# Performance work log

Measured on AMD Instinct MI355X. Metric: run time of the kernel, lower is better.

## Reference

```python
import jax, jax.numpy as jnp
import numpy as np

N = 50000       # nodes
E_RAND = 800000 # random edges (avg degree ~16)
K = 64          # edges touching `node`; setup_inputs guarantees exactly K
F = 64          # num_node_features
C = 64          # conv_channels


def setup_inputs() -> dict:
    key = jax.random.key(0)
    ks = jax.random.split(key, 6)
    x = jax.random.normal(ks[0], (N, F), dtype=jnp.float32)
    # random edges avoiding node 0 so exactly the K prepended edges touch node 0
    src = jax.random.randint(ks[1], (E_RAND,), 1, N, dtype=jnp.int64)
    dst = jax.random.randint(ks[2], (E_RAND,), 1, N, dtype=jnp.int64)
    ksrc = jnp.zeros((K,), dtype=jnp.int64)
    kdst = jnp.arange(1, K + 1, dtype=jnp.int64)
    edge_index = jnp.stack([jnp.concatenate([ksrc, src]),
                            jnp.concatenate([kdst, dst])])  # [2, K+E_RAND]
    W1 = jax.random.normal(ks[3], (F, C), jnp.float32) / np.float32(np.sqrt(F))
    b1 = jnp.zeros((C,), jnp.float32)
    W2 = jax.random.normal(ks[4], (C, C), jnp.float32) / np.float32(np.sqrt(C))
    b2 = jnp.zeros((C,), jnp.float32)
    Wr = jax.random.normal(ks[5], (C, 1), jnp.float32) / np.float32(np.sqrt(C))
    br = jnp.zeros((1,), jnp.float32)
    return {"x": x, "edge_index": edge_index, "node": 0,
            "W1": W1, "b1": b1, "W2": W2, "b2": b2, "Wr": Wr, "br": br}


def gcn_conv(x, src, dst, W, b):
    """PyG GCNConv with self-loops already appended to (src, dst).
    out[v] = sum_{(u,v)} deg(u)^-1/2 * deg(v)^-1/2 * (x @ W)[u] + b
    """
    n = x.shape[0]
    xw = x @ W                                              # [N, C]
    deg = jnp.zeros((n,), xw.dtype).at[dst].add(1.0)        # in-degree incl. self-loop
    dinv = jnp.where(deg > 0, jax.lax.rsqrt(deg), 0.0)
    norm = dinv[src] * dinv[dst]                            # [E]
    out = jax.ops.segment_sum(xw[src] * norm[:, None], dst, num_segments=n)
    return out + b


def reference(x, edge_index, node, W1, b1, W2, b2, Wr, br):
    n = x.shape[0]
    loop = jnp.arange(n, dtype=edge_index.dtype)
    src = jnp.concatenate([edge_index[0], loop])  # add self loops (GCNConv default)
    dst = jnp.concatenate([edge_index[1], loop])
    h = jax.nn.relu(gcn_conv(x, src, dst, W1, b1))
    h = jax.nn.relu(gcn_conv(h, src, dst, W2, b2))
    # edges incident to `node` (setup guarantees exactly K such edges)
    s0, d0 = edge_index[0], edge_index[1]
    mask = (s0 == node) | (d0 == node)
    idx = jnp.nonzero(mask, size=K)[0]
    s, d = s0[idx], d0[idx]
    targets = jnp.where(s == node, d, s)  # self-loop (s==d==node) -> node
    score = h[targets] @ Wr + br          # [K, 1]
    score = jax.nn.softmax(score, axis=0)
    return score[:, 0], targets
```

## Files before the change

kernel.cpp:

```cpp
#include <hip/hip_runtime.h>
#include <math.h>

#define KK 64
#define CAP 64
#define NF 4160
#define BMW 1568

__device__ __forceinline__ int fnode_of(int i, const int* tsorted, const int* towner,
                                        const int* tcnt2, const int* tslots) {
    int tp = i / 65, j = i % 65;
    if (j == 0) return tsorted[tp];
    int own = towner[tp];
    int c = tcnt2[own]; if (c > CAP) c = CAP;
    return (j - 1 < c) ? tslots[own * CAP + (j - 1)] : -1;
}

__global__ __launch_bounds__(256) void k_find(const int* __restrict__ ei, int E,
                                              const int* __restrict__ nodep,
                                              int4* __restrict__ zbase, int zcount4,
                                              int* __restrict__ tcount,
                                              int* __restrict__ tpairs) {
    int idx = blockIdx.x * 256 + threadIdx.x;
    if (idx < zcount4) zbase[idx] = make_int4(0, 0, 0, 0);
    int node = nodep[0];
    int n4 = E >> 2;
    if (idx < n4) {
        int4 ss = ((const int4*)ei)[idx];
        int4 dd = ((const int4*)(ei + E))[idx];
        int s[4] = {ss.x, ss.y, ss.z, ss.w};
        int d[4] = {dd.x, dd.y, dd.z, dd.w};
#pragma unroll
        for (int k = 0; k < 4; k++) {
            if (s[k] == node || d[k] == node) {
                int q = atomicAdd(tcount, 1);
                if (q < KK) { int e = idx * 4 + k; tpairs[2 * q] = e; tpairs[2 * q + 1] = (s[k] == node) ? d[k] : s[k]; }
            }
        }
    }
    if (idx == 0) {
        for (int e = n4 * 4; e < E; e++) {
            int s = ei[e], d = ei[E + e];
            if (s == node || d == node) {
                int q = atomicAdd(tcount, 1);
                if (q < KK) { tpairs[2 * q] = e; tpairs[2 * q + 1] = (s == node) ? d : s; }
            }
        }
    }
}

__global__ __launch_bounds__(256) void k_collect_t(const int* __restrict__ ei, int E,
                                                   const int* __restrict__ tpairs,
                                                   int* __restrict__ cnt,
                                                   int* __restrict__ tcnt2,
                                                   int* __restrict__ tslots,
                                                   int* __restrict__ fmapRow,
                                                   int* __restrict__ tsorted_g,
                                                   int* __restrict__ towner_g) {
    __shared__ unsigned int bmask[BMW];
    __shared__ int tnode[KK];
    __shared__ int eidx[KK], tgt[KK], srt[KK];
    int tid = threadIdx.x;
    for (int i = tid; i < BMW; i += 256) bmask[i] = 0u;
    if (tid < KK) { eidx[tid] = tpairs[2 * tid]; tgt[tid] = tpairs[2 * tid + 1]; }
    __syncthreads();
    if (tid < KK) {
        int rank = 0;
        for (int j = 0; j < KK; j++) rank += (eidx[j] < eidx[tid]) ? 1 : 0;
        srt[rank] = tgt[tid];
    }
    __syncthreads();
    if (tid < KK) {
        int mynode = srt[tid];
        int owner = tid;
        for (int j = 0; j < tid; j++) if (srt[j] == mynode) { owner = j; break; }
        tnode[tid] = (owner == tid) ? mynode : -1;
        if (owner == tid) atomicOr(&bmask[mynode >> 5], 1u << (mynode & 31));
        if (blockIdx.x == 0) {
            tsorted_g[tid] = mynode; towner_g[tid] = owner;
            if (owner == tid) atomicCAS(&fmapRow[mynode], 0, tid * 65 + 0 + 1);
        }
    }
    __syncthreads();
    int n4 = E >> 2;
    for (int idx = blockIdx.x * 256 + tid; idx < n4; idx += gridDim.x * 256) {
        int4 ss = ((const int4*)ei)[idx];
        int4 dd = ((const int4*)(ei + E))[idx];
        int s[4] = {ss.x, ss.y, ss.z, ss.w};
        int d[4] = {dd.x, dd.y, dd.z, dd.w};
        atomicAdd(&cnt[d[0]], 1);
        atomicAdd(&cnt[d[1]], 1);
#pragma unroll
        for (int k = 0; k < 4; k++) {
            if ((bmask[d[k] >> 5] >> (d[k] & 31)) & 1u) {
                int f = 0;
                for (int j = 0; j < KK; j++) if (tnode[j] == d[k]) { f = j + 1; break; }
                if (f) {
                    int p = atomicAdd(&tcnt2[f - 1], 1);
                    if (p < CAP) {
                        tslots[(f - 1) * CAP + p] = s[k];
                        atomicCAS(&fmapRow[s[k]], 0, (f - 1) * 65 + (p + 1) + 1);
                    }
                }
            }
        }
    }
    if (blockIdx.x == 0 && tid == 0) {
        for (int e = n4 * 4; e < E; e++) {
            int d = ei[E + e];
            atomicAdd(&cnt[d], 1);
            if ((bmask[d >> 5] >> (d & 31)) & 1u) {
                int f = 0;
                for (int j = 0; j < KK; j++) if (tnode[j] == d) { f = j + 1; break; }
                if (f) {
                    int p = atomicAdd(&tcnt2[f - 1], 1);
                    if (p < CAP) {
                        tslots[(f - 1) * CAP + p] = ei[e];
                        atomicCAS(&fmapRow[ei[e]], 0, (f - 1) * 65 + (p + 1) + 1);
                    }
                }
            }
        }
    }
}

__global__ __launch_bounds__(256) void k_collect_f(const int* __restrict__ ei, int E,
                                                   const int* __restrict__ fmapRow,
                                                   int* __restrict__ cnt,
                                                   int* __restrict__ fcnt,
                                                   int* __restrict__ fslots,
                                                   const int* __restrict__ tsorted,
                                                   const int* __restrict__ towner,
                                                   const int* __restrict__ tcnt2,
                                                   const int* __restrict__ tslots,
                                                   int* __restrict__ ownerCount,
                                                   int2* __restrict__ owners) {
    int idx = blockIdx.x * 256 + threadIdx.x;
    if (idx < NF) {
        int u = fnode_of(idx, tsorted, towner, tcnt2, tslots);
        if (u >= 0 && fmapRow[u] == idx + 1) {
            int p = atomicAdd(ownerCount, 1);
            owners[p] = make_int2(idx, u);
        }
    }
    int n4 = E >> 2;
    if (idx < n4) {
        int4 ss = ((const int4*)ei)[idx];
        int4 dd = ((const int4*)(ei + E))[idx];
        atomicAdd(&cnt[dd.z], 1);
        atomicAdd(&cnt[dd.w], 1);
        int r0 = fmapRow[dd.x], r1 = fmapRow[dd.y], r2 = fmapRow[dd.z], r3 = fmapRow[dd.w];
        if (r0) { int p = atomicAdd(&fcnt[r0 - 1], 1); if (p < CAP) fslots[(size_t)(r0 - 1) * CAP + p] = ss.x; }
        if (r1) { int p = atomicAdd(&fcnt[r1 - 1], 1); if (p < CAP) fslots[(size_t)(r1 - 1) * CAP + p] = ss.y; }
        if (r2) { int p = atomicAdd(&fcnt[r2 - 1], 1); if (p < CAP) fslots[(size_t)(r2 - 1) * CAP + p] = ss.z; }
        if (r3) { int p = atomicAdd(&fcnt[r3 - 1], 1); if (p < CAP) fslots[(size_t)(r3 - 1) * CAP + p] = ss.w; }
    }
    if (idx == 0) {
        for (int e = n4 * 4; e < E; e++) {
            int r = fmapRow[ei[E + e]];
            if (r) { int p = atomicAdd(&fcnt[r - 1], 1); if (p < CAP) fslots[(size_t)(r - 1) * CAP + p] = ei[e]; }
        }
    }
}

__global__ __launch_bounds__(256) void k_layer1(const float* __restrict__ x,
                                                const int2* __restrict__ owners,
                                                const int* __restrict__ ownerCount,
                                                const int* __restrict__ cnt,
                                                const int* __restrict__ fcnt,
                                                const int* __restrict__ fslots,
                                                const float* __restrict__ W1,
                                                const float* __restrict__ b1,
                                                float* __restrict__ h1s) {
    __shared__ __align__(16) float W1s[64 * 64];
    int tid = threadIdx.x;
    int nown = ownerCount[0];
    int ngrp = (nown + 3) >> 2;
    if ((int)blockIdx.x >= ngrp) return;
    for (int j = tid; j < 1024; j += 256) ((float4*)W1s)[j] = ((const float4*)W1)[j];
    __syncthreads();
    int lane = tid & 63;
    for (int g = blockIdx.x; g < ngrp; g += gridDim.x) {
        int idx = g * 4 + (tid >> 6);
        if (idx >= nown) continue;
        int2 ou = owners[idx];
        int i = ou.x, u = ou.y;
        float du = rsqrtf((float)(cnt[u] + 1));
        float acc = du * x[(size_t)u * 64 + lane];
        int c = fcnt[i]; if (c > CAP) c = CAP;
        const int* sl = fslots + (size_t)i * CAP;
        int k = 0;
        for (; k + 4 <= c; k += 4) {
            int u0 = sl[k], u1 = sl[k + 1], u2 = sl[k + 2], u3 = sl[k + 3];
            float f0 = rsqrtf((float)(cnt[u0] + 1));
            float f1 = rsqrtf((float)(cnt[u1] + 1));
            float f2 = rsqrtf((float)(cnt[u2] + 1));
            float f3 = rsqrtf((float)(cnt[u3] + 1));
            acc += f0 * x[(size_t)u0 * 64 + lane] + f1 * x[(size_t)u1 * 64 + lane]
                 + f2 * x[(size_t)u2 * 64 + lane] + f3 * x[(size_t)u3 * 64 + lane];
        }
        for (; k < c; k++) {
            int uu = sl[k];
            acc += rsqrtf((float)(cnt[uu] + 1)) * x[(size_t)uu * 64 + lane];
        }
        float z = du * acc;
        float h = 0.f;
#pragma unroll
        for (int f = 0; f < 64; f++) h += __shfl(z, f) * W1s[f * 64 + lane];
        h = fmaxf(h + b1[lane], 0.f);
        h1s[(size_t)i * 64 + lane] = du * h;
    }
}

__global__ __launch_bounds__(64) void k_score2(const float* __restrict__ h1s,
                                               const int* __restrict__ tsorted,
                                               const int* __restrict__ towner,
                                               const int* __restrict__ tcnt2,
                                               const int* __restrict__ tslots,
                                               const int* __restrict__ fmapRow,
                                               const int* __restrict__ cnt,
                                               const float* __restrict__ W2,
                                               const float* __restrict__ b2,
                                               const float* __restrict__ Wr,
                                               float* __restrict__ sc,
                                               int* __restrict__ done,
                                               float* __restrict__ out) {
    int tp = blockIdx.x;
    int lane = threadIdx.x;
    int t = tsorted[tp];
    float dt = rsqrtf((float)(cnt[t] + 1));
    int own = towner[tp];
    int c = tcnt2[own]; if (c > CAP) c = CAP;
    const int* sl = tslots + own * CAP;
    float z = h1s[(size_t)(fmapRow[t] - 1) * 64 + lane];
#pragma unroll 8
    for (int j = 0; j < c; j++) {
        int u = sl[j];
        int row = fmapRow[u] - 1;
        z += h1s[(size_t)row * 64 + lane];
    }
    z *= dt;
    float acc = 0.f;
#pragma unroll
    for (int f = 0; f < 64; f++) acc += __shfl(z, f) * W2[f * 64 + lane];
    float h2 = fmaxf(acc + b2[lane], 0.f);
    float p = h2 * Wr[lane];
#pragma unroll
    for (int off = 32; off >= 1; off >>= 1) p += __shfl_xor(p, off);
    int last = 0;
    if (lane == 0) {
        __hip_atomic_store(&sc[tp], p, __ATOMIC_RELEASE, __HIP_MEMORY_SCOPE_AGENT);
        last = (__hip_atomic_fetch_add(done, 1, __ATOMIC_ACQ_REL, __HIP_MEMORY_SCOPE_AGENT) == KK - 1) ? 1 : 0;
    }
    last = __shfl(last, 0);
    if (last) {
        float s = __hip_atomic_load(&sc[lane], __ATOMIC_ACQUIRE, __HIP_MEMORY_SCOPE_AGENT);
        float m = s;
#pragma unroll
        for (int off = 32; off >= 1; off >>= 1) m = fmaxf(m, __shfl_xor(m, off));
        float e = __expf(s - m);
        float ssum = e;
#pragma unroll
        for (int off = 32; off >= 1; off >>= 1) ssum += __shfl_xor(ssum, off);
        out[lane] = e / ssum;
        out[KK + lane] = (float)tsorted[lane];
    }
}

extern "C" void kernel_launch(void* const* d_in, const int* in_sizes, int n_in,
                              void* d_out, int out_size, void* d_ws, size_t ws_size,
                              hipStream_t stream) {
    const float* x  = (const float*)d_in[0];
    const int*   ei = (const int*)d_in[1];
    const int*   nodep = (const int*)d_in[2];
    const float* W1 = (const float*)d_in[3];
    const float* b1 = (const float*)d_in[4];
    const float* W2 = (const float*)d_in[5];
    const float* b2 = (const float*)d_in[6];
    const float* Wr = (const float*)d_in[7];
    const float* br = (const float*)d_in[8];
    float* out = (float*)d_out;
    (void)br; (void)n_in; (void)out_size; (void)ws_size;

    int N = in_sizes[0] / 64;
    int E = in_sizes[1] / 2;

    char* w = (char*)d_ws;
    int* cnt     = (int*)w; w += (size_t)N * 4;
    int* fmapRow = (int*)w; w += (size_t)N * 4;
    int* fcnt    = (int*)w; w += (size_t)NF * 4;
    int* tcnt2   = (int*)w; w += KK * 4;
    int* aux     = (int*)w; w += 16;
    int zcount4 = (2 * N + NF + KK + 4) / 4;
    int* tcount = (int*)w; w += 16;
    int* tpairs  = (int*)w; w += 2 * KK * 4;
    int* tsorted = (int*)w; w += KK * 4;
    int* towner  = (int*)w; w += KK * 4;
    int* tslots  = (int*)w; w += (size_t)KK * CAP * 4;
    int2* owners = (int2*)w; w += (size_t)NF * 8;
    int* fslots  = (int*)w; w += (size_t)NF * CAP * 4;
    float* h1s   = (float*)w; w += (size_t)NF * 64 * 4;
    float* sc    = (float*)w; w += KK * 4;

    hipMemsetAsync(tcount, 0, 16, stream);

    int n4 = E >> 2;
    int ebl = (n4 + 255) / 256;
    k_find<<<ebl, 256, 0, stream>>>(ei, E, nodep, (int4*)cnt, zcount4, tcount, tpairs);
    k_collect_t<<<512, 256, 0, stream>>>(ei, E, tpairs, cnt, tcnt2, tslots, fmapRow, tsorted, towner);
    k_collect_f<<<ebl, 256, 0, stream>>>(ei, E, fmapRow, cnt, fcnt, fslots,
                                         tsorted, towner, tcnt2, tslots, &aux[0], owners);
    k_layer1<<<288, 256, 0, stream>>>(x, owners, &aux[0], cnt, fcnt, fslots, W1, b1, h1s);
    k_score2<<<KK, 64, 0, stream>>>(h1s, tsorted, towner, tcnt2, tslots, fmapRow,
                                    cnt, W2, b2, Wr, sc, &aux[1], out);
}
```

Measured before the change: 145.7 us.

## Move degree counting into find pass and load sources only on hits

The in-degree atomic counting, which used to be split across the collect kernels, is now done entirely in the first edge scan. Workspace zeroing moves from an in-kernel int4 store to a single hipMemsetAsync, and the tcount counter now lives in the aux area. The two collect kernels no longer read the source-index half of edge_index in bulk; they load a source only when a destination matches. This cuts edge-stream bandwidth in the later passes, but puts all the scattered counting atomics in one kernel and adds a memset call.

New measurement: 159.4 us. 1.09x slower.

```diff
diff --git a/kernel.cpp b/kernel.cpp
--- a/kernel.cpp
+++ b/kernel.cpp
@@ -17,11 +17,10 @@
 
 __global__ __launch_bounds__(256) void k_find(const int* __restrict__ ei, int E,
                                               const int* __restrict__ nodep,
-                                              int4* __restrict__ zbase, int zcount4,
+                                              int* __restrict__ cnt,
                                               int* __restrict__ tcount,
                                               int* __restrict__ tpairs) {
     int idx = blockIdx.x * 256 + threadIdx.x;
-    if (idx < zcount4) zbase[idx] = make_int4(0, 0, 0, 0);
     int node = nodep[0];
     int n4 = E >> 2;
     if (idx < n4) {
@@ -29,6 +28,10 @@
         int4 dd = ((const int4*)(ei + E))[idx];
         int s[4] = {ss.x, ss.y, ss.z, ss.w};
         int d[4] = {dd.x, dd.y, dd.z, dd.w};
+        atomicAdd(&cnt[d[0]], 1);
+        atomicAdd(&cnt[d[1]], 1);
+        atomicAdd(&cnt[d[2]], 1);
+        atomicAdd(&cnt[d[3]], 1);
 #pragma unroll
         for (int k = 0; k < 4; k++) {
             if (s[k] == node || d[k] == node) {
@@ -40,6 +43,7 @@
     if (idx == 0) {
         for (int e = n4 * 4; e < E; e++) {
             int s = ei[e], d = ei[E + e];
+            atomicAdd(&cnt[d], 1);
             if (s == node || d == node) {
                 int q = atomicAdd(tcount, 1);
                 if (q < KK) { tpairs[2 * q] = e; tpairs[2 * q + 1] = (s == node) ? d : s; }
@@ -50,7 +54,6 @@
 
 __global__ __launch_bounds__(256) void k_collect_t(const int* __restrict__ ei, int E,
                                                    const int* __restrict__ tpairs,
-                                                   int* __restrict__ cnt,
                                                    int* __restrict__ tcnt2,
                                                    int* __restrict__ tslots,
                                                    int* __restrict__ fmapRow,
@@ -83,22 +86,19 @@
     __syncthreads();
     int n4 = E >> 2;
     for (int idx = blockIdx.x * 256 + tid; idx < n4; idx += gridDim.x * 256) {
-        int4 ss = ((const int4*)ei)[idx];
         int4 dd = ((const int4*)(ei + E))[idx];
-        int s[4] = {ss.x, ss.y, ss.z, ss.w};
         int d[4] = {dd.x, dd.y, dd.z, dd.w};
-        atomicAdd(&cnt[d[0]], 1);
-        atomicAdd(&cnt[d[1]], 1);
 #pragma unroll
         for (int k = 0; k < 4; k++) {
             if ((bmask[d[k] >> 5] >> (d[k] & 31)) & 1u) {
                 int f = 0;
                 for (int j = 0; j < KK; j++) if (tnode[j] == d[k]) { f = j + 1; break; }
                 if (f) {
+                    int s = ei[idx * 4 + k];
                     int p = atomicAdd(&tcnt2[f - 1], 1);
                     if (p < CAP) {
-                        tslots[(f - 1) * CAP + p] = s[k];
-                        atomicCAS(&fmapRow[s[k]], 0, (f - 1) * 65 + (p + 1) + 1);
+                        tslots[(f - 1) * CAP + p] = s;
+                        atomicCAS(&fmapRow[s], 0, (f - 1) * 65 + (p + 1) + 1);
                     }
                 }
             }
@@ -107,15 +107,15 @@
     if (blockIdx.x == 0 && tid == 0) {
         for (int e = n4 * 4; e < E; e++) {
             int d = ei[E + e];
-            atomicAdd(&cnt[d], 1);
             if ((bmask[d >> 5] >> (d & 31)) & 1u) {
                 int f = 0;
                 for (int j = 0; j < KK; j++) if (tnode[j] == d) { f = j + 1; break; }
                 if (f) {
+                    int s = ei[e];
                     int p = atomicAdd(&tcnt2[f - 1], 1);
                     if (p < CAP) {
-                        tslots[(f - 1) * CAP + p] = ei[e];
-                        atomicCAS(&fmapRow[ei[e]], 0, (f - 1) * 65 + (p + 1) + 1);
+                        tslots[(f - 1) * CAP + p] = s;
+                        atomicCAS(&fmapRow[s], 0, (f - 1) * 65 + (p + 1) + 1);
                     }
                 }
             }
@@ -125,7 +125,6 @@
 
 __global__ __launch_bounds__(256) void k_collect_f(const int* __restrict__ ei, int E,
                                                    const int* __restrict__ fmapRow,
-                                                   int* __restrict__ cnt,
                                                    int* __restrict__ fcnt,
                                                    int* __restrict__ fslots,
                                                    const int* __restrict__ tsorted,
@@ -144,20 +143,22 @@
     }
     int n4 = E >> 2;
     if (idx < n4) {
-        int4 ss = ((const int4*)ei)[idx];
         int4 dd = ((const int4*)(ei + E))[idx];
-        atomicAdd(&cnt[dd.z], 1);
-        atomicAdd(&cnt[dd.w], 1);
         int r0 = fmapRow[dd.x], r1 = fmapRow[dd.y], r2 = fmapRow[dd.z], r3 = fmapRow[dd.w];
-        if (r0) { int p = atomicAdd(&fcnt[r0 - 1], 1); if (p < CAP) fslots[(size_t)(r0 - 1) * CAP + p] = ss.x; }
-        if (r1) { int p = atomicAdd(&fcnt[r1 - 1], 1); if (p < CAP) fslots[(size_t)(r1 - 1) * CAP + p] = ss.y; }
-        if (r2) { int p = atomicAdd(&fcnt[r2 - 1], 1); if (p < CAP) fslots[(size_t)(r2 - 1) * CAP + p] = ss.z; }
-        if (r3) { int p = atomicAdd(&fcnt[r3 - 1], 1); if (p < CAP) fslots[(size_t)(r3 - 1) * CAP + p] = ss.w; }
+        if (r0) { int s = ei[idx * 4 + 0]; int p = atomicAdd(&fcnt[r0 - 1], 1);
+                  if (p < CAP) fslots[(size_t)(r0 - 1) * CAP + p] = s; }
+        if (r1) { int s = ei[idx * 4 + 1]; int p = atomicAdd(&fcnt[r1 - 1], 1);
+                  if (p < CAP) fslots[(size_t)(r1 - 1) * CAP + p] = s; }
+        if (r2) { int s = ei[idx * 4 + 2]; int p = atomicAdd(&fcnt[r2 - 1], 1);
+                  if (p < CAP) fslots[(size_t)(r2 - 1) * CAP + p] = s; }
+        if (r3) { int s = ei[idx * 4 + 3]; int p = atomicAdd(&fcnt[r3 - 1], 1);
+                  if (p < CAP) fslots[(size_t)(r3 - 1) * CAP + p] = s; }
     }
     if (idx == 0) {
         for (int e = n4 * 4; e < E; e++) {
             int r = fmapRow[ei[E + e]];
-            if (r) { int p = atomicAdd(&fcnt[r - 1], 1); if (p < CAP) fslots[(size_t)(r - 1) * CAP + p] = ei[e]; }
+            if (r) { int s = ei[e]; int p = atomicAdd(&fcnt[r - 1], 1);
+                     if (p < CAP) fslots[(size_t)(r - 1) * CAP + p] = s; }
         }
     }
 }
@@ -290,8 +291,7 @@
     int* fcnt    = (int*)w; w += (size_t)NF * 4;
     int* tcnt2   = (int*)w; w += KK * 4;
     int* aux     = (int*)w; w += 16;
-    int zcount4 = (2 * N + NF + KK + 4) / 4;
-    int* tcount = (int*)w; w += 16;
+    size_t zbytes = (size_t)(2 * N + NF + KK) * 4 + 16;
     int* tpairs  = (int*)w; w += 2 * KK * 4;
     int* tsorted = (int*)w; w += KK * 4;
     int* towner  = (int*)w; w += KK * 4;
@@ -301,13 +301,13 @@
     float* h1s   = (float*)w; w += (size_t)NF * 64 * 4;
     float* sc    = (float*)w; w += KK * 4;
 
-    hipMemsetAsync(tcount, 0, 16, stream);
+    hipMemsetAsync(cnt, 0, zbytes, stream);
 
     int n4 = E >> 2;
     int ebl = (n4 + 255) / 256;
-    k_find<<<ebl, 256, 0, stream>>>(ei, E, nodep, (int4*)cnt, zcount4, tcount, tpairs);
-    k_collect_t<<<512, 256, 0, stream>>>(ei, E, tpairs, cnt, tcnt2, tslots, fmapRow, tsorted, towner);
-    k_collect_f<<<ebl, 256, 0, stream>>>(ei, E, fmapRow, cnt, fcnt, fslots,
+    k_find<<<ebl, 256, 0, stream>>>(ei, E, nodep, cnt, &aux[2], tpairs);
+    k_collect_t<<<512, 256, 0, stream>>>(ei, E, tpairs, tcnt2, tslots, fmapRow, tsorted, towner);
+    k_collect_f<<<ebl, 256, 0, stream>>>(ei, E, fmapRow, fcnt, fslots,
                                          tsorted, towner, tcnt2, tslots, &aux[0], owners);
     k_layer1<<<288, 256, 0, stream>>>(x, owners, &aux[0], cnt, fcnt, fslots, W1, b1, h1s);
     k_score2<<<KK, 64, 0, stream>>>(h1s, tsorted, towner, tcnt2, tslots, fmapRow,
```
